# Kernel tuning notes

Measured on AMD Instinct MI355X. Metric: run time of the kernel, lower is better.

Reference implementation:

```python
import jax, jax.numpy as jnp
import numpy as np

N = 50000
E = 800000
D = 128
L = 2


def setup_inputs() -> dict:
    key = jax.random.key(0)
    k0, k1, k2 = jax.random.split(key, 3)
    x = jax.random.normal(k0, (N, D), dtype=jnp.float32)
    edge_index = jax.random.randint(k1, (2, E), 0, N, dtype=jnp.int64)
    # GCNConv weights: one [D, D] matrix + bias per layer (dim_in -> dim_in)
    W = jax.random.normal(k2, (L, D, D), dtype=jnp.float32) * (1.0 / np.sqrt(D))
    b = jnp.zeros((L, D), dtype=jnp.float32)
    return {"x": x, "edge_index": edge_index, "W": W, "b": b}


def reference(x, edge_index, W, b):
    """Stacked GCNConv + relu (dropout is identity in eval mode).

    GCNConv: out = D^{-1/2} (A + I) D^{-1/2} (X W) + b, with self-loops added.
    """
    n = x.shape[0]
    loops = jnp.arange(n, dtype=edge_index.dtype)
    src = jnp.concatenate([edge_index[0], loops])  # [E + N]
    dst = jnp.concatenate([edge_index[1], loops])  # [E + N]
    # Degree (with self-loops) based symmetric normalization
    deg = jax.ops.segment_sum(jnp.ones_like(dst, dtype=x.dtype), dst, num_segments=n)
    dinv = jax.lax.rsqrt(deg)  # deg >= 1 thanks to self-loops
    coef = (dinv[src] * dinv[dst])[:, None]  # [E + N, 1]

    num_layers = W.shape[0]
    for i in range(num_layers):
        h = x @ W[i]  # transform first, as PyG GCNConv does
        x = jax.ops.segment_sum(h[src] * coef, dst, num_segments=n) + b[i]
        x = jax.nn.relu(x)
        # F.dropout with training=False is identity
    return x
```

## Files before the change

kernel.cpp:

```cpp
#include <hip/hip_runtime.h>
#include <hip/hip_fp16.h>


#define D 128
#define SCAN_B 256
#define WP 136
#define ABI 6

typedef _Float16 half8 __attribute__((ext_vector_type(8)));
typedef float floatx4 __attribute__((ext_vector_type(4)));


__global__ void count_kernel(const int* __restrict__ dst, int* degInt,
                             int* __restrict__ rank, int e) {
    int i = blockIdx.x * blockDim.x + threadIdx.x;
    if (i < e) rank[i] = atomicAdd(&degInt[dst[i]], 1);
}

__global__ __launch_bounds__(SCAN_B) void scanA_kernel(const int* __restrict__ degInt,
                                                       int* __restrict__ partial, int n) {
    __shared__ int red[SCAN_B / 64];
    int tid = threadIdx.x;
    int i = blockIdx.x * SCAN_B + tid;
    int c = (i < n) ? degInt[i] : 0;
    int s = c;
    for (int off = 32; off > 0; off >>= 1) s += __shfl_down(s, off, 64);
    if ((tid & 63) == 0) red[tid >> 6] = s;
    __syncthreads();
    if (tid == 0) {
        int t = 0;
#pragma unroll
        for (int w = 0; w < SCAN_B / 64; ++w) t += red[w];
        partial[blockIdx.x] = t;
    }
}

__global__ __launch_bounds__(256) void scanB_kernel(const int* __restrict__ partial,
                                                    int* __restrict__ blockoff, int nb) {
    __shared__ int sc[256];
    int tid = threadIdx.x;
    int c = (tid < nb) ? partial[tid] : 0;
    sc[tid] = c;
    __syncthreads();
    for (int off = 1; off < 256; off <<= 1) {
        int v = (tid >= off) ? sc[tid - off] : 0;
        __syncthreads();
        sc[tid] += v;
        __syncthreads();
    }
    if (tid <= nb) blockoff[tid] = (tid == 0) ? 0 : sc[tid - 1];
}

__global__ __launch_bounds__(SCAN_B) void scanC_kernel(const int* __restrict__ degInt,
                                                       const int* __restrict__ blockoff,
                                                       int* __restrict__ row_ptr,
                                                       float* __restrict__ dinv,
                                                       int n, int nb) {
    __shared__ int sc[SCAN_B];
    int tid = threadIdx.x;
    int i = blockIdx.x * SCAN_B + tid;
    int c = (i < n) ? degInt[i] : 0;
    sc[tid] = c;
    __syncthreads();
    for (int off = 1; off < SCAN_B; off <<= 1) {
        int v = (tid >= off) ? sc[tid - off] : 0;
        __syncthreads();
        sc[tid] += v;
        __syncthreads();
    }
    if (i < n) {
        int base = blockoff[blockIdx.x] + sc[tid] - c;
        row_ptr[i] = base;
        dinv[i] = rsqrtf((float)(c + 1));
    }
    if (blockIdx.x == 0 && tid == 0) row_ptr[n] = blockoff[nb];
}

__global__ __launch_bounds__(256) void cvtw_kernel(const float* __restrict__ W,
                                                   __half* __restrict__ WhT) {
    int id = blockIdx.x * blockDim.x + threadIdx.x;
    int l = id >> 14;
    int rem = id & 16383;
    int f = rem >> 7;
    int k = rem & 127;
    WhT[id] = __float2half(W[l * 16384 + k * 128 + f]);
}


__device__ inline void gemm_body(int bid, int tid,
                                 const float* __restrict__ Xf,
                                 const __half* __restrict__ Xh,
                                 const __half* __restrict__ WhT,
                                 __half* __restrict__ Hh, int n, int fromFloat,
                                 _Float16* wlds) {
#pragma unroll
    for (int q = 0; q < 8; ++q) {
        int idx = tid + q * 256;
        int row = idx >> 4;
        int col8 = (idx & 15) * 8;
        const uint2* gsrc = (const uint2*)(WhT + row * 128 + col8);
        uint2 a = gsrc[0];
        uint2 b = gsrc[1];
        uint2* ldst = (uint2*)(wlds + row * WP + col8);
        ldst[0] = a;
        ldst[1] = b;
    }
    __syncthreads();

    const int wave = tid >> 6;
    const int lane = tid & 63;
    const int m = lane & 15;
    const int quad = lane >> 4;

    const int node = bid * 64 + wave * 16 + m;
    const int node_ld = node < n ? node : (n - 1);

    half8 bfr[4];
    if (fromFloat) {
#pragma unroll
        for (int k = 0; k < 4; ++k) {
            const float4* p = (const float4*)(Xf + (size_t)node_ld * 128 + k * 32 + quad * 8);
            float4 lo = p[0];
            float4 hi = p[1];
            half8 h;
            h[0] = (_Float16)lo.x; h[1] = (_Float16)lo.y;
            h[2] = (_Float16)lo.z; h[3] = (_Float16)lo.w;
            h[4] = (_Float16)hi.x; h[5] = (_Float16)hi.y;
            h[6] = (_Float16)hi.z; h[7] = (_Float16)hi.w;
            bfr[k] = h;
        }
    } else {
#pragma unroll
        for (int k = 0; k < 4; ++k) {
            bfr[k] = *(const half8*)(Xh + (size_t)node_ld * 128 + k * 32 + quad * 8);
        }
    }

    floatx4 acc[8];
#pragma unroll
    for (int f = 0; f < 8; ++f) acc[f] = (floatx4){0.f, 0.f, 0.f, 0.f};

#pragma unroll
    for (int f = 0; f < 8; ++f) {
#pragma unroll
        for (int k = 0; k < 4; ++k) {
            half8 a = *(const half8*)(wlds + (f * 16 + m) * WP + k * 32 + quad * 8);
            acc[f] = __builtin_amdgcn_mfma_f32_16x16x32_f16(a, bfr[k], acc[f], 0, 0, 0);
        }
    }

    if (node < n) {
#pragma unroll
        for (int f = 0; f < 8; ++f) {
            __half2 p0 = __floats2half2_rn(acc[f][0], acc[f][1]);
            __half2 p1 = __floats2half2_rn(acc[f][2], acc[f][3]);
            uint2 pk;
            pk.x = *(unsigned int*)&p0;
            pk.y = *(unsigned int*)&p1;
            *(uint2*)(Hh + (size_t)node * 128 + f * 16 + quad * 4) = pk;
        }
    }
}

__device__ inline void fill_body(int i,
                                 const int* __restrict__ src,
                                 const int* __restrict__ dst,
                                 const int* __restrict__ rank,
                                 const int* __restrict__ row_ptr,
                                 const float* __restrict__ dinv,
                                 int2* __restrict__ recs, int e) {
    if (i < e) {
        int d = dst[i];
        int s = src[i];
        int pos = row_ptr[d] + rank[i];
        int2 rec;
        rec.x = s;
        rec.y = __float_as_int(dinv[s] * dinv[d]);
        recs[pos] = rec;
    }
}


__global__ __launch_bounds__(256) void gemmfill_kernel(const float* __restrict__ Xf,
                                                       const __half* __restrict__ WhT,
                                                       __half* __restrict__ Hh, int n, int nbg,
                                                       const int* __restrict__ src,
                                                       const int* __restrict__ dst,
                                                       const int* __restrict__ rank,
                                                       const int* __restrict__ row_ptr,
                                                       const float* __restrict__ dinv,
                                                       int2* __restrict__ recs, int e) {
    __shared__ _Float16 wlds[128 * WP];
    int bid = blockIdx.x;
    int tid = threadIdx.x;
    if (bid < nbg) {
        gemm_body(bid, tid, Xf, nullptr, WhT, Hh, n, 1, wlds);
    } else {
        fill_body((bid - nbg) * 256 + tid, src, dst, rank, row_ptr, dinv, recs, e);
    }
}

__global__ __launch_bounds__(256) void gemm_f16in_kernel(const __half* __restrict__ Xh,
                                                         const __half* __restrict__ WhT,
                                                         __half* __restrict__ Hh, int n) {
    __shared__ _Float16 wlds[128 * WP];
    gemm_body(blockIdx.x, threadIdx.x, nullptr, Xh, WhT, Hh, n, 0, wlds);
}


__device__ inline void unpack8(uint4 u, float* f) {
    union { unsigned int x; __half2 h; } a, b, c, d;
    a.x = u.x; b.x = u.y; c.x = u.z; d.x = u.w;
    float2 f0 = __half22float2(a.h);
    float2 f1 = __half22float2(b.h);
    float2 f2 = __half22float2(c.h);
    float2 f3 = __half22float2(d.h);
    f[0] = f0.x; f[1] = f0.y; f[2] = f1.x; f[3] = f1.y;
    f[4] = f2.x; f[5] = f2.y; f[6] = f3.x; f[7] = f3.y;
}

__global__ __launch_bounds__(256) void agg_kernel(const __half* __restrict__ H,
                                                  const int2* __restrict__ recs,
                                                  const int* __restrict__ row_ptr,
                                                  const float* __restrict__ dinv,
                                                  const float* __restrict__ bias,
                                                  float* __restrict__ YF,
                                                  __half* __restrict__ YH,
                                                  int n, int writeHalf) {
    int wave = threadIdx.x >> 6;
    int lane = threadIdx.x & 63;
    int v = blockIdx.x * 4 + wave;
    if (v >= n) return;

    const int qw = lane >> 4;
    const int fl = lane & 15;
    const uint4* H16 = (const uint4*)H;

    float acc[8];
    {
        float di = dinv[v];
        float selfc = (qw == 0) ? di * di : 0.f;
        uint4 hv = H16[(size_t)v * 16 + fl];
        float f[8]; unpack8(hv, f);
#pragma unroll
        for (int t = 0; t < 8; ++t) acc[t] = f[t] * selfc;
    }

    int e0 = row_ptr[v];
    int e1 = row_ptr[v + 1];
    int e = e0;
    for (; e + 4 * ABI <= e1; e += 4 * ABI) {
        int2 r[ABI]; uint4 hu[ABI];
#pragma unroll
        for (int j = 0; j < ABI; ++j) r[j] = recs[e + 4 * j + qw];
#pragma unroll
        for (int j = 0; j < ABI; ++j) hu[j] = H16[(size_t)r[j].x * 16 + fl];
#pragma unroll
        for (int j = 0; j < ABI; ++j) {
            float c = __int_as_float(r[j].y);
            float f[8]; unpack8(hu[j], f);
#pragma unroll
            for (int t = 0; t < 8; ++t) acc[t] = fmaf(f[t], c, acc[t]);
        }
    }
    if (e < e1) {
        int2 r[ABI]; uint4 hu[ABI]; bool act[ABI];
#pragma unroll
        for (int j = 0; j < ABI; ++j) {
            int idx = e + 4 * j + qw;
            act[j] = idx < e1;
            if (act[j]) r[j] = recs[idx];
        }
#pragma unroll
        for (int j = 0; j < ABI; ++j) {
            if (act[j]) hu[j] = H16[(size_t)r[j].x * 16 + fl];
        }
#pragma unroll
        for (int j = 0; j < ABI; ++j) {
            if (act[j]) {
                float c = __int_as_float(r[j].y);
                float f[8]; unpack8(hu[j], f);
#pragma unroll
                for (int t = 0; t < 8; ++t) acc[t] = fmaf(f[t], c, acc[t]);
            }
        }
    }

#pragma unroll
    for (int t = 0; t < 8; ++t) {
        acc[t] += __shfl_xor(acc[t], 16);
        acc[t] += __shfl_xor(acc[t], 32);
    }

    if (qw == 0) {
        const float4* B4 = (const float4*)bias;
        float4 b0 = B4[fl * 2];
        float4 b1 = B4[fl * 2 + 1];
        float o[8];
        o[0] = fmaxf(acc[0] + b0.x, 0.f);
        o[1] = fmaxf(acc[1] + b0.y, 0.f);
        o[2] = fmaxf(acc[2] + b0.z, 0.f);
        o[3] = fmaxf(acc[3] + b0.w, 0.f);
        o[4] = fmaxf(acc[4] + b1.x, 0.f);
        o[5] = fmaxf(acc[5] + b1.y, 0.f);
        o[6] = fmaxf(acc[6] + b1.z, 0.f);
        o[7] = fmaxf(acc[7] + b1.w, 0.f);
        if (writeHalf) {
            __half2 p0 = __floats2half2_rn(o[0], o[1]);
            __half2 p1 = __floats2half2_rn(o[2], o[3]);
            __half2 p2 = __floats2half2_rn(o[4], o[5]);
            __half2 p3 = __floats2half2_rn(o[6], o[7]);
            uint4 pk;
            pk.x = *(unsigned int*)&p0;
            pk.y = *(unsigned int*)&p1;
            pk.z = *(unsigned int*)&p2;
            pk.w = *(unsigned int*)&p3;
            ((uint4*)YH)[(size_t)v * 16 + fl] = pk;
        } else {
            float4* Y4 = (float4*)YF;
            Y4[(size_t)v * 32 + fl * 2]     = make_float4(o[0], o[1], o[2], o[3]);
            Y4[(size_t)v * 32 + fl * 2 + 1] = make_float4(o[4], o[5], o[6], o[7]);
        }
    }
}


extern "C" void kernel_launch(void* const* d_in, const int* in_sizes, int n_in,
                              void* d_out, int out_size, void* d_ws, size_t ws_size,
                              hipStream_t stream) {
    const float* x = (const float*)d_in[0];
    const int* ei = (const int*)d_in[1];
    const float* W = (const float*)d_in[2];
    const float* b = (const float*)d_in[3];
    float* out = (float*)d_out;

    const int N = in_sizes[0] / D;
    const int E = in_sizes[1] / 2;

    const int* src = ei;
    const int* dst = ei + E;

    int* wsi = (int*)d_ws;
    float* wsf = (float*)d_ws;
    const size_t o_deg  = 0;
    const size_t o_dinv = o_deg + 50000;
    const size_t o_rp   = o_dinv + 50000;
    const size_t o_part = o_rp + 50016;
    const size_t o_boff = o_part + 256;
    const size_t o_rank = o_boff + 256;
    const size_t o_rec  = o_rank + 800000;
    const size_t o_h    = o_rec + 1600000;
    const size_t o_wht  = o_h + 3200000;
    const size_t o_y1h  = o_wht + 16384;

    int* degInt  = wsi + o_deg;
    float* dinv  = wsf + o_dinv;
    int* row_ptr = wsi + o_rp;
    int* partial = wsi + o_part;
    int* blockoff= wsi + o_boff;
    int* rank    = wsi + o_rank;
    int2* recs   = (int2*)(wsi + o_rec);
    __half* h    = (__half*)(wsi + o_h);
    __half* wht  = (__half*)(wsi + o_wht);
    __half* y1h  = (__half*)(wsi + o_y1h);

    const int nb_e = (E + 255) / 256;
    const int nb_s = (N + SCAN_B - 1) / SCAN_B;
    const int nb_g = (N + 63) / 64;
    const int nb_a = (N + 3) / 4;

    hipMemsetAsync(degInt, 0, (size_t)50000 * sizeof(int), stream);
    count_kernel<<<nb_e, 256, 0, stream>>>(dst, degInt, rank, E);
    scanA_kernel<<<nb_s, SCAN_B, 0, stream>>>(degInt, partial, N);
    scanB_kernel<<<1, 256, 0, stream>>>(partial, blockoff, nb_s);
    scanC_kernel<<<nb_s, SCAN_B, 0, stream>>>(degInt, blockoff, row_ptr, dinv, N, nb_s);
    cvtw_kernel<<<128, 256, 0, stream>>>(W, wht);
    gemmfill_kernel<<<nb_g + nb_e, 256, 0, stream>>>(x, wht, h, N, nb_g,
                                                     src, dst, rank, row_ptr, dinv, recs, E);
    agg_kernel<<<nb_a, 256, 0, stream>>>(h, recs, row_ptr, dinv, b, nullptr, y1h, N, 1);
    gemm_f16in_kernel<<<nb_g, 256, 0, stream>>>(y1h, wht + 16384, h, N);
    agg_kernel<<<nb_a, 256, 0, stream>>>(h, recs, row_ptr, dinv, b + D, out, nullptr, N, 0);
}
```

Baseline: 239.8 us.

## Privatize degree counters into 8 copies and fuse weight conversion into scan

The degree histogram is split into 8 private copies, chosen by block index, to reduce atomic contention in the count kernel. A per-copy exclusive base is computed in the first scan stage so the CSR fill can still place each edge deterministically. The weight fp16 transpose kernel is merged into that scan kernel to save one launch. The cost is a memset eight times larger, extra reads and writes of the 8-way arrays, and one more gather in the fill step.

```diff
diff --git a/kernel.cpp b/kernel.cpp
--- a/kernel.cpp
+++ b/kernel.cpp
@@ -11,27 +11,47 @@
 typedef float floatx4 __attribute__((ext_vector_type(4)));
 
 
-__global__ void count_kernel(const int* __restrict__ dst, int* degInt,
-                             int* __restrict__ rank, int e) {
+__global__ void count_kernel(const int* __restrict__ dst, int* deg8,
+                             int* __restrict__ rank, int e, int n) {
     int i = blockIdx.x * blockDim.x + threadIdx.x;
-    if (i < e) rank[i] = atomicAdd(&degInt[dst[i]], 1);
-}
-
-__global__ __launch_bounds__(SCAN_B) void scanA_kernel(const int* __restrict__ degInt,
-                                                       int* __restrict__ partial, int n) {
-    __shared__ int red[SCAN_B / 64];
+    int c = (blockIdx.x & 7) * n;
+    if (i < e) rank[i] = atomicAdd(&deg8[c + dst[i]], 1);
+}
+
+__global__ __launch_bounds__(256) void scanA_cvtw_kernel(const int* __restrict__ deg8,
+                                                         int* __restrict__ degT,
+                                                         int* __restrict__ base8,
+                                                         int* __restrict__ partial,
+                                                         int n, int nbs,
+                                                         const float* __restrict__ W,
+                                                         __half* __restrict__ WhT) {
+    __shared__ int red[4];
     int tid = threadIdx.x;
-    int i = blockIdx.x * SCAN_B + tid;
-    int c = (i < n) ? degInt[i] : 0;
-    int s = c;
-    for (int off = 32; off > 0; off >>= 1) s += __shfl_down(s, off, 64);
-    if ((tid & 63) == 0) red[tid >> 6] = s;
-    __syncthreads();
-    if (tid == 0) {
-        int t = 0;
-#pragma unroll
-        for (int w = 0; w < SCAN_B / 64; ++w) t += red[w];
-        partial[blockIdx.x] = t;
+    int bid = blockIdx.x;
+    if (bid < nbs) {
+        int i = bid * 256 + tid;
+        int tot = 0;
+        if (i < n) {
+            int run = 0;
+#pragma unroll
+            for (int c = 0; c < 8; ++c) {
+                base8[c * n + i] = run;
+                run += deg8[c * n + i];
+            }
+            degT[i] = run;
+            tot = run;
+        }
+        for (int off = 32; off > 0; off >>= 1) tot += __shfl_down(tot, off, 64);
+        if ((tid & 63) == 0) red[tid >> 6] = tot;
+        __syncthreads();
+        if (tid == 0) partial[bid] = red[0] + red[1] + red[2] + red[3];
+    } else {
+        int id = (bid - nbs) * 256 + tid;
+        int l = id >> 14;
+        int rem = id & 16383;
+        int f = rem >> 7;
+        int k = rem & 127;
+        WhT[id] = __float2half(W[l * 16384 + k * 128 + f]);
     }
 }
 
@@ -51,7 +71,7 @@
     if (tid <= nb) blockoff[tid] = (tid == 0) ? 0 : sc[tid - 1];
 }
 
-__global__ __launch_bounds__(SCAN_B) void scanC_kernel(const int* __restrict__ degInt,
+__global__ __launch_bounds__(SCAN_B) void scanC_kernel(const int* __restrict__ degT,
                                                        const int* __restrict__ blockoff,
                                                        int* __restrict__ row_ptr,
                                                        float* __restrict__ dinv,
@@ -59,7 +79,7 @@
     __shared__ int sc[SCAN_B];
     int tid = threadIdx.x;
     int i = blockIdx.x * SCAN_B + tid;
-    int c = (i < n) ? degInt[i] : 0;
+    int c = (i < n) ? degT[i] : 0;
     sc[tid] = c;
     __syncthreads();
     for (int off = 1; off < SCAN_B; off <<= 1) {
@@ -74,16 +94,6 @@
         dinv[i] = rsqrtf((float)(c + 1));
     }
     if (blockIdx.x == 0 && tid == 0) row_ptr[n] = blockoff[nb];
-}
-
-__global__ __launch_bounds__(256) void cvtw_kernel(const float* __restrict__ W,
-                                                   __half* __restrict__ WhT) {
-    int id = blockIdx.x * blockDim.x + threadIdx.x;
-    int l = id >> 14;
-    int rem = id & 16383;
-    int f = rem >> 7;
-    int k = rem & 127;
-    WhT[id] = __float2half(W[l * 16384 + k * 128 + f]);
 }
 
 
@@ -167,12 +177,14 @@
                                  const int* __restrict__ dst,
                                  const int* __restrict__ rank,
                                  const int* __restrict__ row_ptr,
+                                 const int* __restrict__ base8,
                                  const float* __restrict__ dinv,
-                                 int2* __restrict__ recs, int e) {
+                                 int2* __restrict__ recs, int e, int n) {
     if (i < e) {
         int d = dst[i];
         int s = src[i];
-        int pos = row_ptr[d] + rank[i];
+        int c = (i >> 8) & 7;
+        int pos = row_ptr[d] + base8[c * n + d] + rank[i];
         int2 rec;
         rec.x = s;
         rec.y = __float_as_int(dinv[s] * dinv[d]);
@@ -188,6 +200,7 @@
                                                        const int* __restrict__ dst,
                                                        const int* __restrict__ rank,
                                                        const int* __restrict__ row_ptr,
+                                                       const int* __restrict__ base8,
                                                        const float* __restrict__ dinv,
                                                        int2* __restrict__ recs, int e) {
     __shared__ _Float16 wlds[128 * WP];
@@ -196,7 +209,7 @@
     if (bid < nbg) {
         gemm_body(bid, tid, Xf, nullptr, WhT, Hh, n, 1, wlds);
     } else {
-        fill_body((bid - nbg) * 256 + tid, src, dst, rank, row_ptr, dinv, recs, e);
+        fill_body((bid - nbg) * 256 + tid, src, dst, rank, row_ptr, base8, dinv, recs, e, n);
     }
 }
 
@@ -342,22 +355,26 @@
 
     int* wsi = (int*)d_ws;
     float* wsf = (float*)d_ws;
-    const size_t o_deg  = 0;
-    const size_t o_dinv = o_deg + 50000;
+    const size_t o_deg8 = 0;
+    const size_t o_degT = o_deg8 + 400000;
+    const size_t o_dinv = o_degT + 50000;
     const size_t o_rp   = o_dinv + 50000;
     const size_t o_part = o_rp + 50016;
     const size_t o_boff = o_part + 256;
-    const size_t o_rank = o_boff + 256;
+    const size_t o_b8   = o_boff + 256;
+    const size_t o_rank = o_b8 + 400000;
     const size_t o_rec  = o_rank + 800000;
     const size_t o_h    = o_rec + 1600000;
     const size_t o_wht  = o_h + 3200000;
     const size_t o_y1h  = o_wht + 16384;
 
-    int* degInt  = wsi + o_deg;
+    int* deg8    = wsi + o_deg8;
+    int* degT    = wsi + o_degT;
     float* dinv  = wsf + o_dinv;
     int* row_ptr = wsi + o_rp;
     int* partial = wsi + o_part;
     int* blockoff= wsi + o_boff;
+    int* base8   = wsi + o_b8;
     int* rank    = wsi + o_rank;
     int2* recs   = (int2*)(wsi + o_rec);
     __half* h    = (__half*)(wsi + o_h);
@@ -369,14 +386,15 @@
     const int nb_g = (N + 63) / 64;
     const int nb_a = (N + 3) / 4;
 
-    hipMemsetAsync(degInt, 0, (size_t)50000 * sizeof(int), stream);
-    count_kernel<<<nb_e, 256, 0, stream>>>(dst, degInt, rank, E);
-    scanA_kernel<<<nb_s, SCAN_B, 0, stream>>>(degInt, partial, N);
+    hipMemsetAsync(deg8, 0, (size_t)8 * 50000 * sizeof(int), stream);
+    count_kernel<<<nb_e, 256, 0, stream>>>(dst, deg8, rank, E, N);
+    scanA_cvtw_kernel<<<nb_s + 128, 256, 0, stream>>>(deg8, degT, base8, partial,
+                                                      N, nb_s, W, wht);
     scanB_kernel<<<1, 256, 0, stream>>>(partial, blockoff, nb_s);
-    scanC_kernel<<<nb_s, SCAN_B, 0, stream>>>(degInt, blockoff, row_ptr, dinv, N, nb_s);
-    cvtw_kernel<<<128, 256, 0, stream>>>(W, wht);
+    scanC_kernel<<<nb_s, SCAN_B, 0, stream>>>(degT, blockoff, row_ptr, dinv, N, nb_s);
     gemmfill_kernel<<<nb_g + nb_e, 256, 0, stream>>>(x, wht, h, N, nb_g,
-                                                     src, dst, rank, row_ptr, dinv, recs, E);
+                                                     src, dst, rank, row_ptr, base8,
+                                                     dinv, recs, E);
     agg_kernel<<<nb_a, 256, 0, stream>>>(h, recs, row_ptr, dinv, b, nullptr, y1h, N, 1);
     gemm_f16in_kernel<<<nb_g, 256, 0, stream>>>(y1h, wht + 16384, h, N);
     agg_kernel<<<nb_a, 256, 0, stream>>>(h, recs, row_ptr, dinv, b + D, out, nullptr, N, 0);
```

Result: no change. 238.4 us, median of 2 (-0.6%).
